# Kernel optimization log

Hardware: AMD Instinct MI355X
Metric: run time of the kernel (lower is better)

## Reference

```python
import jax, jax.numpy as jnp
import numpy as np

V = 8192        # variants
NREF = 262144   # total ref reads
NALT = 131072   # total alt reads
F_READ = 11     # tensors.NUM_READ_FEATURES
F_INFO = 9      # tensors.NUM_INFO_FEATURES
H = 256         # hidden width
MAX_ALT = 10


def setup_inputs() -> dict:
    key = jax.random.key(0)
    ks = jax.random.split(key, 24)
    p = lambda k, shp: (jax.random.normal(k, shp, dtype=jnp.float32) * 0.05)
    inp = {
        "reads": jax.random.normal(ks[0], (NREF + NALT, F_READ), dtype=jnp.float32),
        "info": jax.random.normal(ks[1], (V, F_INFO), dtype=jnp.float32),
        "ref_seg_ids": jnp.sort(jax.random.randint(ks[2], (NREF,), 0, V, dtype=jnp.int32)),
        "alt_seg_ids": jnp.sort(jax.random.randint(ks[3], (NALT,), 0, V, dtype=jnp.int32)),
        "variant_types": jax.random.randint(ks[4], (V,), 0, 3, dtype=jnp.int32),
        # phi: [F_READ, H, H]
        "phi_W0": p(ks[5], (F_READ, H)), "phi_b0": p(ks[6], (H,)),
        "phi_W1": p(ks[7], (H, H)), "phi_b1": p(ks[8], (H,)),
        # omega: [F_INFO, H]
        "om_W0": p(ks[9], (F_INFO, H)), "om_b0": p(ks[10], (H,)),
        # rho: [3H, H, H]
        "rho_W0": p(ks[11], (3 * H, H)), "rho_b0": p(ks[12], (H,)),
        "rho_W1": p(ks[13], (H, H)), "rho_b1": p(ks[14], (H,)),
        # 3 output MLPs, stacked: [H,H] -> [H,1]
        "out_W1": p(ks[15], (3, H, H)), "out_b1": p(ks[16], (3, H)),
        "out_W2": p(ks[17], (3, H, 1)), "out_b2": p(ks[18], (3, 1)),
        # calibration
        "conf": jnp.sqrt(jnp.arange(0, MAX_ALT + 1, dtype=jnp.float32)),
        "max_logit": jnp.array(10.0, dtype=jnp.float32),
    }
    return inp


def _seg_mean(x, seg_ids, num_segments):
    sums = jax.ops.segment_sum(x, seg_ids, num_segments=num_segments)
    counts = jax.ops.segment_sum(jnp.ones((x.shape[0],), x.dtype), seg_ids, num_segments=num_segments)
    return sums / jnp.maximum(counts, 1.0)[:, None], counts


def reference(reads, info, ref_seg_ids, alt_seg_ids, variant_types,
              phi_W0, phi_b0, phi_W1, phi_b1, om_W0, om_b0,
              rho_W0, rho_b0, rho_W1, rho_b1,
              out_W1, out_b1, out_W2, out_b2, conf, max_logit):
    lrelu = jax.nn.leaky_relu
    # phi MLP (leaky_relu between layers, none after last), then sigmoid
    h = lrelu(reads @ phi_W0 + phi_b0)
    phi_reads = jax.nn.sigmoid(h @ phi_W1 + phi_b1)          # [N, H]
    ref_reads = phi_reads[:NREF]
    alt_reads = phi_reads[NREF:]
    ref_means, _ = _seg_mean(ref_reads, ref_seg_ids, V)       # [V, H]
    alt_means, alt_counts = _seg_mean(alt_reads, alt_seg_ids, V)
    omega_info = jax.nn.sigmoid(info @ om_W0 + om_b0)         # [V, H]
    concat = jnp.concatenate([ref_means, alt_means, omega_info], axis=1)  # [V, 3H]
    agg = lrelu(concat @ rho_W0 + rho_b0) @ rho_W1 + rho_b1   # [V, H]
    # per-variant-type output MLPs, select by variant type
    o = lrelu(jnp.einsum('vd,tde->tve', agg, out_W1) + out_b1[:, None, :])
    outs = (jnp.einsum('tve,teo->tvo', o, out_W2) + out_b2[:, None, :])[:, :, 0]  # [3, V]
    logits = jnp.take_along_axis(outs, variant_types[None, :].astype(jnp.int32), axis=0)[0]
    # calibration
    trunc = jnp.minimum(alt_counts.astype(jnp.int32), MAX_ALT)
    logits = logits * conf[trunc]
    return max_logit * jnp.tanh(logits / max_logit)
```

## Files before the change

kernel.cpp:

```cpp
#include <hip/hip_runtime.h>
#include <cmath>

#define V 8192
#define NREF 262144
#define NALT 131072
#define NREADS (NREF + NALT)
#define FR 11
#define FI 9
#define HH 256
#define MAX_ALT 10

#define TILE_R 64
#define TILE_V 32

#define HPITCH 264
#define RBPITCH 40
#define CPITCH 776
#define APITCH 264

typedef short bf16x8 __attribute__((ext_vector_type(8)));
typedef float f32x4  __attribute__((ext_vector_type(4)));

__device__ __forceinline__ float sigmoidf_(float x) {
    return __builtin_amdgcn_rcpf(1.0f + __expf(-x));
}
__device__ __forceinline__ float lrelu_(float x) {
    return x > 0.0f ? x : 0.01f * x;
}
__device__ __forceinline__ unsigned short f2bf_(float f) {
    unsigned int u = __float_as_uint(f);
    u += 0x7FFFu + ((u >> 16) & 1u);
    return (unsigned short)(u >> 16);
}
__device__ __forceinline__ float bf2f_(unsigned short b) {
    return __uint_as_float(((unsigned int)b) << 16);
}

__global__ __launch_bounds__(256) void prep_kernel(
    const float* __restrict__ phi_W1, const float* __restrict__ rho_W0,
    const float* __restrict__ rho_W1, const float* __restrict__ out_W1,
    const float* __restrict__ phi_W0,
    unsigned short* __restrict__ w1t_phi, unsigned short* __restrict__ w0t,
    unsigned short* __restrict__ w1rt, unsigned short* __restrict__ whT,
    unsigned short* __restrict__ w0pT)
{
    __shared__ unsigned short sT[32][33];
    const int b = blockIdx.x;
    const int t = threadIdx.x;
    if (b < 512) {
        const float* src; unsigned short* dst; int R, C, bx, by;
        if (b < 64)       { src = phi_W1; dst = w1t_phi; R = 256; C = 256; bx = b & 7; by = b >> 3; }
        else if (b < 256) { int i = b - 64;  src = rho_W0; dst = w0t;  R = 768; C = 256; bx = i & 7; by = i >> 3; }
        else if (b < 320) { int i = b - 256; src = rho_W1; dst = w1rt; R = 256; C = 256; bx = i & 7; by = i >> 3; }
        else              { int i = b - 320; int z = i >> 6; i &= 63;
                            src = out_W1 + (size_t)z * HH * HH; dst = whT + (size_t)z * HH * HH;
                            R = 256; C = 256; bx = i & 7; by = i >> 3; }
        const int tx = t & 31, ty = t >> 5;
        const int r0 = by * 32, c0 = bx * 32;
#pragma unroll
        for (int k = 0; k < 4; k++)
            sT[ty + k * 8][tx] = f2bf_(src[(size_t)(r0 + ty + k * 8) * C + c0 + tx]);
        __syncthreads();
#pragma unroll
        for (int k = 0; k < 4; k++)
            dst[(size_t)(c0 + ty + k * 8) * R + r0 + tx] = sT[tx][ty + k * 8];
    } else {
        const int idx = (b - 512) * 256 + t;
        const int c = idx >> 5, k = idx & 31;
        unsigned short v = 0;
        if (k < FR) v = f2bf_(phi_W0[k * HH + c]);
        else if (k >= 16 && k < 16 + FR) v = f2bf_(phi_W0[(k - 16) * HH + c]);
        w0pT[idx] = v;
    }
}

__global__ __launch_bounds__(256, 4) void phi_seg_kernel(
    const float* __restrict__ reads,
    const int* __restrict__ ref_ids, const int* __restrict__ alt_ids,
    const unsigned short* __restrict__ w0pT, const float* __restrict__ b0,
    const unsigned short* __restrict__ w1t, const float* __restrict__ b1,
    float* __restrict__ ref_sums, float* __restrict__ alt_sums,
    int* __restrict__ ref_cnt, int* __restrict__ alt_cnt)
{
    __shared__ __align__(16) unsigned short sH[TILE_R * HPITCH];
    __shared__ __align__(16) unsigned short sRB[TILE_R * RBPITCH];

    const int t  = threadIdx.x;
    const int r0 = blockIdx.x * TILE_R;
    const bool is_ref = (r0 < NREF);
    const int* seg_ids = is_ref ? ref_ids : alt_ids;
    const int sbase    = is_ref ? r0 : (r0 - NREF);
    float* sums = is_ref ? ref_sums : alt_sums;
    int*   cnts = is_ref ? ref_cnt  : alt_cnt;

    {
        const int row = t >> 2, q = t & 3;
        const float* rp = reads + (size_t)(r0 + row) * FR;
        unsigned short o[8];
        if (q == 0) {
#pragma unroll
            for (int j = 0; j < 8; j++) o[j] = f2bf_(rp[j]);
        } else if (q == 1) {
#pragma unroll
            for (int j = 0; j < 8; j++) o[j] = (j < 3) ? f2bf_(rp[8 + j]) : 0;
        } else if (q == 2) {
#pragma unroll
            for (int j = 0; j < 8; j++) {
                float f = rp[j];
                o[j] = f2bf_(f - bf2f_(f2bf_(f)));
            }
        } else {
#pragma unroll
            for (int j = 0; j < 8; j++) {
                if (j < 3) { float f = rp[8 + j]; o[j] = f2bf_(f - bf2f_(f2bf_(f))); }
                else o[j] = 0;
            }
        }
        uint4 pk;
        pk.x = (unsigned int)o[0] | ((unsigned int)o[1] << 16);
        pk.y = (unsigned int)o[2] | ((unsigned int)o[3] << 16);
        pk.z = (unsigned int)o[4] | ((unsigned int)o[5] << 16);
        pk.w = (unsigned int)o[6] | ((unsigned int)o[7] << 16);
        *(uint4*)&sRB[row * RBPITCH + q * 8] = pk;
    }
    __syncthreads();

    const int wv   = t >> 6;
    const int lane = t & 63;
    const int lrow = lane & 15;
    const int quad = lane >> 4;

    bf16x8 aw[4], br[4];
#pragma unroll
    for (int cm = 0; cm < 4; cm++)
        aw[cm] = *(const bf16x8*)(w0pT + ((wv * 64 + cm * 16 + lrow) << 5) + quad * 8);
#pragma unroll
    for (int rt = 0; rt < 4; rt++)
        br[rt] = *(const bf16x8*)&sRB[(rt * 16 + lrow) * RBPITCH + quad * 8];

    f32x4 c1[4][4];
#pragma unroll
    for (int cm = 0; cm < 4; cm++)
#pragma unroll
        for (int rt = 0; rt < 4; rt++)
            c1[cm][rt] = __builtin_amdgcn_mfma_f32_16x16x32_bf16(
                aw[cm], br[rt], (f32x4){0.f, 0.f, 0.f, 0.f}, 0, 0, 0);

#pragma unroll
    for (int cm = 0; cm < 4; cm++) {
        const float4 bias = *(const float4*)(b0 + wv * 64 + cm * 16 + quad * 4);
#pragma unroll
        for (int rt = 0; rt < 4; rt++) {
            const int r = rt * 16 + lrow;
            unsigned int p01 =
                (unsigned int)f2bf_(lrelu_(c1[cm][rt][0] + bias.x)) |
                ((unsigned int)f2bf_(lrelu_(c1[cm][rt][1] + bias.y)) << 16);
            unsigned int p23 =
                (unsigned int)f2bf_(lrelu_(c1[cm][rt][2] + bias.z)) |
                ((unsigned int)f2bf_(lrelu_(c1[cm][rt][3] + bias.w)) << 16);
            uint2 pk = {p01, p23};
            *(uint2*)&sH[r * HPITCH + wv * 64 + cm * 16 + quad * 4] = pk;
        }
    }
    __syncthreads();

    f32x4 acc[4][4];
#pragma unroll
    for (int mt = 0; mt < 4; mt++)
#pragma unroll
        for (int nt = 0; nt < 4; nt++)
            acc[mt][nt] = (f32x4){0.f, 0.f, 0.f, 0.f};

#pragma unroll
    for (int kk = 0; kk < 8; kk++) {
        bf16x8 am[4], bn[4];
#pragma unroll
        for (int mt = 0; mt < 4; mt++)
            am[mt] = *(const bf16x8*)&sH[(mt * 16 + lrow) * HPITCH + kk * 32 + quad * 8];
#pragma unroll
        for (int nt = 0; nt < 4; nt++)
            bn[nt] = *(const bf16x8*)(w1t + (size_t)(wv * 64 + nt * 16 + lrow) * HH + kk * 32 + quad * 8);
#pragma unroll
        for (int mt = 0; mt < 4; mt++)
#pragma unroll
            for (int nt = 0; nt < 4; nt++)
                acc[mt][nt] = __builtin_amdgcn_mfma_f32_16x16x32_bf16(
                    am[mt], bn[nt], acc[mt][nt], 0, 0, 0);
    }

#pragma unroll
    for (int nt = 0; nt < 4; nt++) {
        const float bb = b1[wv * 64 + nt * 16 + lrow];
#pragma unroll
        for (int mt = 0; mt < 4; mt++)
#pragma unroll
            for (int r = 0; r < 4; r++)
                acc[mt][nt][r] = sigmoidf_(acc[mt][nt][r] + bb);
    }

    const int myseg = seg_ids[sbase + lane];
    const int prev  = __shfl_up(myseg, 1);
    const bool flag = (lane == 0) || (myseg != prev);
    unsigned long long m = __ballot(flag);

    while (m) {
        const int start = (int)__builtin_ctzll(m);
        const unsigned long long m2 = m & (m - 1);
        const int end = m2 ? (int)__builtin_ctzll(m2) : 64;
        m = m2;
        const int seg = __shfl(myseg, start);

        float msk[4][4];
#pragma unroll
        for (int mt = 0; mt < 4; mt++)
#pragma unroll
            for (int r = 0; r < 4; r++) {
                const int row = mt * 16 + quad * 4 + r;
                msk[mt][r] = (row >= start && row < end) ? 1.0f : 0.0f;
            }
#pragma unroll
        for (int nt = 0; nt < 4; nt++) {
            float s = 0.f;
#pragma unroll
            for (int mt = 0; mt < 4; mt++)
#pragma unroll
                for (int r = 0; r < 4; r++)
                    s = fmaf(acc[mt][nt][r], msk[mt][r], s);
            s += __shfl_down(s, 32);
            s += __shfl_down(s, 16);
            if (quad == 0)
                atomicAdd(&sums[(size_t)seg * HH + wv * 64 + nt * 16 + lrow], s);
        }
        if (t == 0) atomicAdd(&cnts[seg], end - start);
    }
}

__global__ __launch_bounds__(1024, 1) void rho_mfma_kernel(
    const float* __restrict__ info, const int* __restrict__ vtypes,
    const float* __restrict__ om_W0, const float* __restrict__ om_b0,
    const unsigned short* __restrict__ w0t, const float* __restrict__ rho_b0,
    const unsigned short* __restrict__ w1rt, const float* __restrict__ rho_b1,
    const unsigned short* __restrict__ whT, const float* __restrict__ out_b1,
    const float* __restrict__ out_W2, const float* __restrict__ out_b2,
    const float* __restrict__ conf, const float* __restrict__ max_logit,
    const float* __restrict__ ref_sums, const float* __restrict__ alt_sums,
    const int* __restrict__ ref_cnt, const int* __restrict__ alt_cnt,
    float* __restrict__ out)
{
    __shared__ __align__(16) unsigned short sC[TILE_V * CPITCH];
    __shared__ __align__(16) float sInfo[TILE_V][12];
    __shared__ float sRinvR[TILE_V], sRinvA[TILE_V];
    __shared__ float sPart[16][3][TILE_V];

    unsigned short* sA1  = sC;
    unsigned short* sAgg = sC + TILE_V * APITCH;

    const int t  = threadIdx.x;
    const int v0 = blockIdx.x * TILE_V;

    if (t < TILE_V) {
        sRinvR[t] = __builtin_amdgcn_rcpf(fmaxf((float)ref_cnt[v0 + t], 1.0f));
        sRinvA[t] = __builtin_amdgcn_rcpf(fmaxf((float)alt_cnt[v0 + t], 1.0f));
    }
    for (int idx = t; idx < TILE_V * FI; idx += 1024) {
        int i = idx / FI, k = idx - i * FI;
        sInfo[i][k] = info[(size_t)(v0 + i) * FI + k];
    }
    __syncthreads();

    {
        const int c = t & 255, grp = t >> 8;
        float om0r[FI];
#pragma unroll
        for (int k = 0; k < FI; k++) om0r[k] = om_W0[k * HH + c];
        const float omb = om_b0[c];
#pragma unroll
        for (int ii = 0; ii < 8; ii++) {
            const int i = grp * 8 + ii, v = v0 + i;
            float rm = ref_sums[(size_t)v * HH + c] * sRinvR[i];
            float am = alt_sums[(size_t)v * HH + c] * sRinvA[i];
            float a = omb;
#pragma unroll
            for (int k = 0; k < FI; k++) a = fmaf(sInfo[i][k], om0r[k], a);
            sC[i * CPITCH + c]          = f2bf_(rm);
            sC[i * CPITCH + HH + c]     = f2bf_(am);
            sC[i * CPITCH + 2 * HH + c] = f2bf_(sigmoidf_(a));
        }
    }
    __syncthreads();

    const int wv   = t >> 6;
    const int lane = t & 63;
    const int lrow = lane & 15;
    const int quad = lane >> 4;
    const int ncol = wv * 16 + lrow;

    f32x4 p1[2] = {(f32x4){0.f,0.f,0.f,0.f}, (f32x4){0.f,0.f,0.f,0.f}};
#pragma unroll 4
    for (int kk = 0; kk < 24; kk++) {
        bf16x8 a0 = *(const bf16x8*)&sC[lrow * CPITCH + kk * 32 + quad * 8];
        bf16x8 a1 = *(const bf16x8*)&sC[(16 + lrow) * CPITCH + kk * 32 + quad * 8];
        bf16x8 bn = *(const bf16x8*)(w0t + (size_t)ncol * 768 + kk * 32 + quad * 8);
        p1[0] = __builtin_amdgcn_mfma_f32_16x16x32_bf16(a0, bn, p1[0], 0, 0, 0);
        p1[1] = __builtin_amdgcn_mfma_f32_16x16x32_bf16(a1, bn, p1[1], 0, 0, 0);
    }
    __syncthreads();
    {
        const float bb = rho_b0[ncol];
#pragma unroll
        for (int mt = 0; mt < 2; mt++)
#pragma unroll
            for (int r = 0; r < 4; r++) {
                const int row = mt * 16 + quad * 4 + r;
                sA1[row * APITCH + ncol] = f2bf_(lrelu_(p1[mt][r] + bb));
            }
    }
    __syncthreads();

    f32x4 p2[2] = {(f32x4){0.f,0.f,0.f,0.f}, (f32x4){0.f,0.f,0.f,0.f}};
#pragma unroll
    for (int kk = 0; kk < 8; kk++) {
        bf16x8 a0 = *(const bf16x8*)&sA1[lrow * APITCH + kk * 32 + quad * 8];
        bf16x8 a1 = *(const bf16x8*)&sA1[(16 + lrow) * APITCH + kk * 32 + quad * 8];
        bf16x8 bn = *(const bf16x8*)(w1rt + (size_t)ncol * HH + kk * 32 + quad * 8);
        p2[0] = __builtin_amdgcn_mfma_f32_16x16x32_bf16(a0, bn, p2[0], 0, 0, 0);
        p2[1] = __builtin_amdgcn_mfma_f32_16x16x32_bf16(a1, bn, p2[1], 0, 0, 0);
    }
    {
        const float bb = rho_b1[ncol];
#pragma unroll
        for (int mt = 0; mt < 2; mt++)
#pragma unroll
            for (int r = 0; r < 4; r++) {
                const int row = mt * 16 + quad * 4 + r;
                sAgg[row * APITCH + ncol] = f2bf_(p2[mt][r] + bb);
            }
    }
    __syncthreads();

    bf16x8 aF[8][2];
#pragma unroll
    for (int kk = 0; kk < 8; kk++)
#pragma unroll
        for (int mt = 0; mt < 2; mt++)
            aF[kk][mt] = *(const bf16x8*)&sAgg[(mt * 16 + lrow) * APITCH + kk * 32 + quad * 8];

    for (int h = 0; h < 3; h++) {
        f32x4 p3[2] = {(f32x4){0.f,0.f,0.f,0.f}, (f32x4){0.f,0.f,0.f,0.f}};
#pragma unroll
        for (int kk = 0; kk < 8; kk++) {
            bf16x8 bn = *(const bf16x8*)(whT + ((size_t)h * HH + ncol) * HH + kk * 32 + quad * 8);
            p3[0] = __builtin_amdgcn_mfma_f32_16x16x32_bf16(aF[kk][0], bn, p3[0], 0, 0, 0);
            p3[1] = __builtin_amdgcn_mfma_f32_16x16x32_bf16(aF[kk][1], bn, p3[1], 0, 0, 0);
        }
        const float bb = out_b1[h * HH + ncol];
        const float w2 = out_W2[h * HH + ncol];
#pragma unroll
        for (int mt = 0; mt < 2; mt++)
#pragma unroll
            for (int r = 0; r < 4; r++) {
                float v = lrelu_(p3[mt][r] + bb) * w2;
                v += __shfl_down(v, 8);
                v += __shfl_down(v, 4);
                v += __shfl_down(v, 2);
                v += __shfl_down(v, 1);
                if (lrow == 0) sPart[wv][h][mt * 16 + quad * 4 + r] = v;
            }
    }
    __syncthreads();

    if (t < TILE_V) {
        const int v = v0 + t;
        const int ty = vtypes[v];
        float logit = 0.f;
#pragma unroll
        for (int w = 0; w < 16; w++) logit += sPart[w][ty][t];
        logit += out_b2[ty];
        const int tr = min(alt_cnt[v], MAX_ALT);
        logit *= conf[tr];
        const float ml = max_logit[0];
        out[v] = ml * tanhf(logit / ml);
    }
}

extern "C" void kernel_launch(void* const* d_in, const int* in_sizes, int n_in,
                              void* d_out, int out_size, void* d_ws, size_t ws_size,
                              hipStream_t stream) {
    const float* reads    = (const float*)d_in[0];
    const float* info     = (const float*)d_in[1];
    const int*   ref_ids  = (const int*)d_in[2];
    const int*   alt_ids  = (const int*)d_in[3];
    const int*   vtypes   = (const int*)d_in[4];
    const float* phi_W0   = (const float*)d_in[5];
    const float* phi_b0   = (const float*)d_in[6];
    const float* phi_W1   = (const float*)d_in[7];
    const float* phi_b1   = (const float*)d_in[8];
    const float* om_W0    = (const float*)d_in[9];
    const float* om_b0    = (const float*)d_in[10];
    const float* rho_W0   = (const float*)d_in[11];
    const float* rho_b0   = (const float*)d_in[12];
    const float* rho_W1   = (const float*)d_in[13];
    const float* rho_b1   = (const float*)d_in[14];
    const float* out_W1   = (const float*)d_in[15];
    const float* out_b1   = (const float*)d_in[16];
    const float* out_W2   = (const float*)d_in[17];
    const float* out_b2   = (const float*)d_in[18];
    const float* conf     = (const float*)d_in[19];
    const float* max_lg   = (const float*)d_in[20];
    float* out = (float*)d_out;

    float* ref_sums = (float*)d_ws;
    float* alt_sums = ref_sums + (size_t)V * HH;
    int*   ref_cnt  = (int*)(alt_sums + (size_t)V * HH);
    int*   alt_cnt  = ref_cnt + V;
    unsigned short* w1t_phi = (unsigned short*)(alt_cnt + V);
    unsigned short* w0t     = w1t_phi + (size_t)HH * HH;
    unsigned short* w1rt    = w0t + (size_t)HH * 768;
    unsigned short* whT     = w1rt + (size_t)HH * HH;
    unsigned short* w0pT    = whT + (size_t)3 * HH * HH;

    const size_t zero_bytes = (size_t)2 * V * HH * sizeof(float) + (size_t)2 * V * sizeof(int);
    hipMemsetAsync(d_ws, 0, zero_bytes, stream);

    prep_kernel<<<544, 256, 0, stream>>>(phi_W1, rho_W0, rho_W1, out_W1, phi_W0,
                                         w1t_phi, w0t, w1rt, whT, w0pT);

    phi_seg_kernel<<<NREADS / TILE_R, 256, 0, stream>>>(
        reads, ref_ids, alt_ids, w0pT, phi_b0, w1t_phi, phi_b1,
        ref_sums, alt_sums, ref_cnt, alt_cnt);

    rho_mfma_kernel<<<V / TILE_V, 1024, 0, stream>>>(
        info, vtypes, om_W0, om_b0, w0t, rho_b0, w1rt, rho_b1,
        whT, out_b1, out_W2, out_b2, conf, max_lg,
        ref_sums, alt_sums, ref_cnt, alt_cnt, out);
}
```

Measured before the change: 264.3 us.

## Retile rho kernel to 16 variants per 512-thread block with two columns per wave

The rho/output kernel now handles 16 variants per block with 512 threads, and each wave computes two 16-column N tiles that share one A fragment, instead of two M tiles sharing one B fragment. This doubles the grid to 512 blocks and allows several blocks per CU, aiming to improve occupancy and latency hiding. The cost is that each block re-reads the full weight matrices from global/L2 for half as many variants, so weight traffic roughly doubles. The phi kernel also switches read staging to a row/quarter mapping with fewer branches, and packs bf16 conversions with the hardware paired-conversion intrinsic.

```diff
diff --git a/kernel.cpp b/kernel.cpp
--- a/kernel.cpp
+++ b/kernel.cpp
@@ -1,4 +1,5 @@
 #include <hip/hip_runtime.h>
+#include <hip/hip_bf16.h>
 #include <cmath>
 
 #define V 8192
@@ -11,7 +12,7 @@
 #define MAX_ALT 10
 
 #define TILE_R 64
-#define TILE_V 32
+#define TILE_V 16
 
 #define HPITCH 264
 #define RBPITCH 40
@@ -34,6 +35,11 @@
 }
 __device__ __forceinline__ float bf2f_(unsigned short b) {
     return __uint_as_float(((unsigned int)b) << 16);
+}
+__device__ __forceinline__ unsigned int pk2bf_(float a, float b) {
+    union { __hip_bfloat162 h2; unsigned int u; } cvt;
+    cvt.h2 = __float22bfloat162_rn(make_float2(a, b));
+    return cvt.u;
 }
 
 __global__ __launch_bounds__(256) void prep_kernel(
@@ -94,26 +100,19 @@
     int*   cnts = is_ref ? ref_cnt  : alt_cnt;
 
     {
-        const int row = t >> 2, q = t & 3;
+        const int row = t & 63, q = t >> 6;
         const float* rp = reads + (size_t)(r0 + row) * FR;
+        const int nj = (q & 1) ? 3 : 8;
+        const int cb = (q & 1) ? 8 : 0;
         unsigned short o[8];
-        if (q == 0) {
-#pragma unroll
-            for (int j = 0; j < 8; j++) o[j] = f2bf_(rp[j]);
-        } else if (q == 1) {
-#pragma unroll
-            for (int j = 0; j < 8; j++) o[j] = (j < 3) ? f2bf_(rp[8 + j]) : 0;
-        } else if (q == 2) {
-#pragma unroll
-            for (int j = 0; j < 8; j++) {
-                float f = rp[j];
+#pragma unroll
+        for (int j = 0; j < 8; j++) o[j] = 0;
+        if (q < 2) {
+            for (int j = 0; j < nj; j++) o[j] = f2bf_(rp[cb + j]);
+        } else {
+            for (int j = 0; j < nj; j++) {
+                float f = rp[cb + j];
                 o[j] = f2bf_(f - bf2f_(f2bf_(f)));
-            }
-        } else {
-#pragma unroll
-            for (int j = 0; j < 8; j++) {
-                if (j < 3) { float f = rp[8 + j]; o[j] = f2bf_(f - bf2f_(f2bf_(f))); }
-                else o[j] = 0;
             }
         }
         uint4 pk;
@@ -152,13 +151,9 @@
 #pragma unroll
         for (int rt = 0; rt < 4; rt++) {
             const int r = rt * 16 + lrow;
-            unsigned int p01 =
-                (unsigned int)f2bf_(lrelu_(c1[cm][rt][0] + bias.x)) |
-                ((unsigned int)f2bf_(lrelu_(c1[cm][rt][1] + bias.y)) << 16);
-            unsigned int p23 =
-                (unsigned int)f2bf_(lrelu_(c1[cm][rt][2] + bias.z)) |
-                ((unsigned int)f2bf_(lrelu_(c1[cm][rt][3] + bias.w)) << 16);
-            uint2 pk = {p01, p23};
+            uint2 pk;
+            pk.x = pk2bf_(lrelu_(c1[cm][rt][0] + bias.x), lrelu_(c1[cm][rt][1] + bias.y));
+            pk.y = pk2bf_(lrelu_(c1[cm][rt][2] + bias.z), lrelu_(c1[cm][rt][3] + bias.w));
             *(uint2*)&sH[r * HPITCH + wv * 64 + cm * 16 + quad * 4] = pk;
         }
     }
@@ -209,6 +204,7 @@
         const int end = m2 ? (int)__builtin_ctzll(m2) : 64;
         m = m2;
         const int seg = __shfl(myseg, start);
+        float* srow = sums + (size_t)seg * HH + wv * 64;
 
         float msk[4][4];
 #pragma unroll
@@ -229,13 +225,13 @@
             s += __shfl_down(s, 32);
             s += __shfl_down(s, 16);
             if (quad == 0)
-                atomicAdd(&sums[(size_t)seg * HH + wv * 64 + nt * 16 + lrow], s);
+                atomicAdd(&srow[nt * 16 + lrow], s);
         }
         if (t == 0) atomicAdd(&cnts[seg], end - start);
     }
 }
 
-__global__ __launch_bounds__(1024, 1) void rho_mfma_kernel(
+__global__ __launch_bounds__(512, 4) void rho_mfma_kernel(
     const float* __restrict__ info, const int* __restrict__ vtypes,
     const float* __restrict__ om_W0, const float* __restrict__ om_b0,
     const unsigned short* __restrict__ w0t, const float* __restrict__ rho_b0,
@@ -250,7 +246,7 @@
     __shared__ __align__(16) unsigned short sC[TILE_V * CPITCH];
     __shared__ __align__(16) float sInfo[TILE_V][12];
     __shared__ float sRinvR[TILE_V], sRinvA[TILE_V];
-    __shared__ float sPart[16][3][TILE_V];
+    __shared__ float sPart[8][3][TILE_V];
 
     unsigned short* sA1  = sC;
     unsigned short* sAgg = sC + TILE_V * APITCH;
@@ -262,7 +258,7 @@
         sRinvR[t] = __builtin_amdgcn_rcpf(fmaxf((float)ref_cnt[v0 + t], 1.0f));
         sRinvA[t] = __builtin_amdgcn_rcpf(fmaxf((float)alt_cnt[v0 + t], 1.0f));
     }
-    for (int idx = t; idx < TILE_V * FI; idx += 1024) {
+    for (int idx = t; idx < TILE_V * FI; idx += 512) {
         int i = idx / FI, k = idx - i * FI;
         sInfo[i][k] = info[(size_t)(v0 + i) * FI + k];
     }
@@ -293,79 +289,75 @@
     const int lane = t & 63;
     const int lrow = lane & 15;
     const int quad = lane >> 4;
-    const int ncol = wv * 16 + lrow;
+    const int nc0  = wv * 32 + lrow;
+    const int nc1  = nc0 + 16;
 
     f32x4 p1[2] = {(f32x4){0.f,0.f,0.f,0.f}, (f32x4){0.f,0.f,0.f,0.f}};
 #pragma unroll 4
     for (int kk = 0; kk < 24; kk++) {
-        bf16x8 a0 = *(const bf16x8*)&sC[lrow * CPITCH + kk * 32 + quad * 8];
-        bf16x8 a1 = *(const bf16x8*)&sC[(16 + lrow) * CPITCH + kk * 32 + quad * 8];
-        bf16x8 bn = *(const bf16x8*)(w0t + (size_t)ncol * 768 + kk * 32 + quad * 8);
-        p1[0] = __builtin_amdgcn_mfma_f32_16x16x32_bf16(a0, bn, p1[0], 0, 0, 0);
-        p1[1] = __builtin_amdgcn_mfma_f32_16x16x32_bf16(a1, bn, p1[1], 0, 0, 0);
+        bf16x8 a  = *(const bf16x8*)&sC[lrow * CPITCH + kk * 32 + quad * 8];
+        bf16x8 b0_ = *(const bf16x8*)(w0t + (size_t)nc0 * 768 + kk * 32 + quad * 8);
+        bf16x8 b1_ = *(const bf16x8*)(w0t + (size_t)nc1 * 768 + kk * 32 + quad * 8);
+        p1[0] = __builtin_amdgcn_mfma_f32_16x16x32_bf16(a, b0_, p1[0], 0, 0, 0);
+        p1[1] = __builtin_amdgcn_mfma_f32_16x16x32_bf16(a, b1_, p1[1], 0, 0, 0);
     }
     __syncthreads();
     {
-        const float bb = rho_b0[ncol];
-#pragma unroll
-        for (int mt = 0; mt < 2; mt++)
-#pragma unroll
-            for (int r = 0; r < 4; r++) {
-                const int row = mt * 16 + quad * 4 + r;
-                sA1[row * APITCH + ncol] = f2bf_(lrelu_(p1[mt][r] + bb));
-            }
+        const float bb0 = rho_b0[nc0], bb1 = rho_b0[nc1];
+#pragma unroll
+        for (int r = 0; r < 4; r++) {
+            const int row = quad * 4 + r;
+            sA1[row * APITCH + nc0] = f2bf_(lrelu_(p1[0][r] + bb0));
+            sA1[row * APITCH + nc1] = f2bf_(lrelu_(p1[1][r] + bb1));
+        }
     }
     __syncthreads();
 
     f32x4 p2[2] = {(f32x4){0.f,0.f,0.f,0.f}, (f32x4){0.f,0.f,0.f,0.f}};
 #pragma unroll
     for (int kk = 0; kk < 8; kk++) {
-        bf16x8 a0 = *(const bf16x8*)&sA1[lrow * APITCH + kk * 32 + quad * 8];
-        bf16x8 a1 = *(const bf16x8*)&sA1[(16 + lrow) * APITCH + kk * 32 + quad * 8];
-        bf16x8 bn = *(const bf16x8*)(w1rt + (size_t)ncol * HH + kk * 32 + quad * 8);
-        p2[0] = __builtin_amdgcn_mfma_f32_16x16x32_bf16(a0, bn, p2[0], 0, 0, 0);
-        p2[1] = __builtin_amdgcn_mfma_f32_16x16x32_bf16(a1, bn, p2[1], 0, 0, 0);
+        bf16x8 a  = *(const bf16x8*)&sA1[lrow * APITCH + kk * 32 + quad * 8];
+        bf16x8 b0_ = *(const bf16x8*)(w1rt + (size_t)nc0 * HH + kk * 32 + quad * 8);
+        bf16x8 b1_ = *(const bf16x8*)(w1rt + (size_t)nc1 * HH + kk * 32 + quad * 8);
+        p2[0] = __builtin_amdgcn_mfma_f32_16x16x32_bf16(a, b0_, p2[0], 0, 0, 0);
+        p2[1] = __builtin_amdgcn_mfma_f32_16x16x32_bf16(a, b1_, p2[1], 0, 0, 0);
     }
     {
-        const float bb = rho_b1[ncol];
-#pragma unroll
-        for (int mt = 0; mt < 2; mt++)
-#pragma unroll
-            for (int r = 0; r < 4; r++) {
-                const int row = mt * 16 + quad * 4 + r;
-                sAgg[row * APITCH + ncol] = f2bf_(p2[mt][r] + bb);
-            }
-    }
-    __syncthreads();
-
-    bf16x8 aF[8][2];
+        const float bb0 = rho_b1[nc0], bb1 = rho_b1[nc1];
+#pragma unroll
+        for (int r = 0; r < 4; r++) {
+            const int row = quad * 4 + r;
+            sAgg[row * APITCH + nc0] = f2bf_(p2[0][r] + bb0);
+            sAgg[row * APITCH + nc1] = f2bf_(p2[1][r] + bb1);
+        }
+    }
+    __syncthreads();
+
+    bf16x8 aF[8];
 #pragma unroll
     for (int kk = 0; kk < 8; kk++)
-#pragma unroll
-        for (int mt = 0; mt < 2; mt++)
-            aF[kk][mt] = *(const bf16x8*)&sAgg[(mt * 16 + lrow) * APITCH + kk * 32 + quad * 8];
+        aF[kk] = *(const bf16x8*)&sAgg[lrow * APITCH + kk * 32 + quad * 8];
 
     for (int h = 0; h < 3; h++) {
         f32x4 p3[2] = {(f32x4){0.f,0.f,0.f,0.f}, (f32x4){0.f,0.f,0.f,0.f}};
 #pragma unroll
         for (int kk = 0; kk < 8; kk++) {
-            bf16x8 bn = *(const bf16x8*)(whT + ((size_t)h * HH + ncol) * HH + kk * 32 + quad * 8);
-            p3[0] = __builtin_amdgcn_mfma_f32_16x16x32_bf16(aF[kk][0], bn, p3[0], 0, 0, 0);
-            p3[1] = __builtin_amdgcn_mfma_f32_16x16x32_bf16(aF[kk][1], bn, p3[1], 0, 0, 0);
-        }
-        const float bb = out_b1[h * HH + ncol];
-        const float w2 = out_W2[h * HH + ncol];
-#pragma unroll
-        for (int mt = 0; mt < 2; mt++)
-#pragma unroll
-            for (int r = 0; r < 4; r++) {
-                float v = lrelu_(p3[mt][r] + bb) * w2;
-                v += __shfl_down(v, 8);
-                v += __shfl_down(v, 4);
-                v += __shfl_down(v, 2);
-                v += __shfl_down(v, 1);
-                if (lrow == 0) sPart[wv][h][mt * 16 + quad * 4 + r] = v;
-            }
+            bf16x8 b0_ = *(const bf16x8*)(whT + ((size_t)h * HH + nc0) * HH + kk * 32 + quad * 8);
+            bf16x8 b1_ = *(const bf16x8*)(whT + ((size_t)h * HH + nc1) * HH + kk * 32 + quad * 8);
+            p3[0] = __builtin_amdgcn_mfma_f32_16x16x32_bf16(aF[kk], b0_, p3[0], 0, 0, 0);
+            p3[1] = __builtin_amdgcn_mfma_f32_16x16x32_bf16(aF[kk], b1_, p3[1], 0, 0, 0);
+        }
+        const float bbA = out_b1[h * HH + nc0], bbB = out_b1[h * HH + nc1];
+        const float w2A = out_W2[h * HH + nc0], w2B = out_W2[h * HH + nc1];
+#pragma unroll
+        for (int r = 0; r < 4; r++) {
+            float v = lrelu_(p3[0][r] + bbA) * w2A + lrelu_(p3[1][r] + bbB) * w2B;
+            v += __shfl_down(v, 8);
+            v += __shfl_down(v, 4);
+            v += __shfl_down(v, 2);
+            v += __shfl_down(v, 1);
+            if (lrow == 0) sPart[wv][h][quad * 4 + r] = v;
+        }
     }
     __syncthreads();
 
@@ -374,7 +366,7 @@
         const int ty = vtypes[v];
         float logit = 0.f;
 #pragma unroll
-        for (int w = 0; w < 16; w++) logit += sPart[w][ty][t];
+        for (int w = 0; w < 8; w++) logit += sPart[w][ty][t];
         logit += out_b2[ty];
         const int tr = min(alt_cnt[v], MAX_ALT);
         logit *= conf[tr];
@@ -429,7 +421,7 @@
         reads, ref_ids, alt_ids, w0pT, phi_b0, w1t_phi, phi_b1,
         ref_sums, alt_sums, ref_cnt, alt_cnt);
 
-    rho_mfma_kernel<<<V / TILE_V, 1024, 0, stream>>>(
+    rho_mfma_kernel<<<V / TILE_V, 512, 0, stream>>>(
         info, vtypes, om_W0, om_b0, w0t, rho_b0, w1rt, rho_b1,
         whT, out_b1, out_W2, out_b2, conf, max_lg,
         ref_sums, alt_sums, ref_cnt, alt_cnt, out);
```

After: 288.4 us. 9.1% more time.

## Double phi row tile to 128 with 512-thread blocks and 32-column wave slices

Applied to the files above, without the earlier changes.

The phi/segment kernel now processes 128 reads per block with 8 waves, each owning 32 output columns across all 128 rows instead of 64 columns over 64 rows. This halves how often the phi_W1 weights are fetched from global memory per read, so weight traffic per read drops. It also switches to a packed bf16x2 conversion intrinsic. In exchange, the shared-memory footprint per block doubles and occupancy per CU may change. The segment reduction is also split into two 64-row passes, which issues more atomics per segment boundary.

```diff
diff --git a/kernel.cpp b/kernel.cpp
--- a/kernel.cpp
+++ b/kernel.cpp
@@ -1,4 +1,5 @@
 #include <hip/hip_runtime.h>
+#include <hip/hip_bf16.h>
 #include <cmath>
 
 #define V 8192
@@ -10,7 +11,7 @@
 #define HH 256
 #define MAX_ALT 10
 
-#define TILE_R 64
+#define TILE_R 128
 #define TILE_V 32
 
 #define HPITCH 264
@@ -34,6 +35,11 @@
 }
 __device__ __forceinline__ float bf2f_(unsigned short b) {
     return __uint_as_float(((unsigned int)b) << 16);
+}
+__device__ __forceinline__ unsigned int pk2bf_(float a, float b) {
+    union { __hip_bfloat162 h2; unsigned int u; } cvt;
+    cvt.h2 = __float22bfloat162_rn(make_float2(a, b));
+    return cvt.u;
 }
 
 __global__ __launch_bounds__(256) void prep_kernel(
@@ -74,7 +80,7 @@
     }
 }
 
-__global__ __launch_bounds__(256, 4) void phi_seg_kernel(
+__global__ __launch_bounds__(512, 2) void phi_seg_kernel(
     const float* __restrict__ reads,
     const int* __restrict__ ref_ids, const int* __restrict__ alt_ids,
     const unsigned short* __restrict__ w0pT, const float* __restrict__ b0,
@@ -94,26 +100,19 @@
     int*   cnts = is_ref ? ref_cnt  : alt_cnt;
 
     {
-        const int row = t >> 2, q = t & 3;
+        const int row = t & 127, q = t >> 7;
         const float* rp = reads + (size_t)(r0 + row) * FR;
+        const int nj = (q & 1) ? 3 : 8;
+        const int cb = (q & 1) ? 8 : 0;
         unsigned short o[8];
-        if (q == 0) {
-#pragma unroll
-            for (int j = 0; j < 8; j++) o[j] = f2bf_(rp[j]);
-        } else if (q == 1) {
-#pragma unroll
-            for (int j = 0; j < 8; j++) o[j] = (j < 3) ? f2bf_(rp[8 + j]) : 0;
-        } else if (q == 2) {
-#pragma unroll
-            for (int j = 0; j < 8; j++) {
-                float f = rp[j];
+#pragma unroll
+        for (int j = 0; j < 8; j++) o[j] = 0;
+        if (q < 2) {
+            for (int j = 0; j < nj; j++) o[j] = f2bf_(rp[cb + j]);
+        } else {
+            for (int j = 0; j < nj; j++) {
+                float f = rp[cb + j];
                 o[j] = f2bf_(f - bf2f_(f2bf_(f)));
-            }
-        } else {
-#pragma unroll
-            for (int j = 0; j < 8; j++) {
-                if (j < 3) { float f = rp[8 + j]; o[j] = f2bf_(f - bf2f_(f2bf_(f))); }
-                else o[j] = 0;
             }
         }
         uint4 pk;
@@ -130,108 +129,101 @@
     const int lrow = lane & 15;
     const int quad = lane >> 4;
 
-    bf16x8 aw[4], br[4];
-#pragma unroll
-    for (int cm = 0; cm < 4; cm++)
-        aw[cm] = *(const bf16x8*)(w0pT + ((wv * 64 + cm * 16 + lrow) << 5) + quad * 8);
-#pragma unroll
-    for (int rt = 0; rt < 4; rt++)
-        br[rt] = *(const bf16x8*)&sRB[(rt * 16 + lrow) * RBPITCH + quad * 8];
-
-    f32x4 c1[4][4];
-#pragma unroll
-    for (int cm = 0; cm < 4; cm++)
-#pragma unroll
-        for (int rt = 0; rt < 4; rt++)
-            c1[cm][rt] = __builtin_amdgcn_mfma_f32_16x16x32_bf16(
-                aw[cm], br[rt], (f32x4){0.f, 0.f, 0.f, 0.f}, 0, 0, 0);
-
-#pragma unroll
-    for (int cm = 0; cm < 4; cm++) {
-        const float4 bias = *(const float4*)(b0 + wv * 64 + cm * 16 + quad * 4);
-#pragma unroll
-        for (int rt = 0; rt < 4; rt++) {
-            const int r = rt * 16 + lrow;
-            unsigned int p01 =
-                (unsigned int)f2bf_(lrelu_(c1[cm][rt][0] + bias.x)) |
-                ((unsigned int)f2bf_(lrelu_(c1[cm][rt][1] + bias.y)) << 16);
-            unsigned int p23 =
-                (unsigned int)f2bf_(lrelu_(c1[cm][rt][2] + bias.z)) |
-                ((unsigned int)f2bf_(lrelu_(c1[cm][rt][3] + bias.w)) << 16);
-            uint2 pk = {p01, p23};
-            *(uint2*)&sH[r * HPITCH + wv * 64 + cm * 16 + quad * 4] = pk;
-        }
-    }
-    __syncthreads();
-
-    f32x4 acc[4][4];
-#pragma unroll
-    for (int mt = 0; mt < 4; mt++)
-#pragma unroll
-        for (int nt = 0; nt < 4; nt++)
+    {
+        bf16x8 br[8];
+#pragma unroll
+        for (int rt = 0; rt < 8; rt++)
+            br[rt] = *(const bf16x8*)&sRB[(rt * 16 + lrow) * RBPITCH + quad * 8];
+
+#pragma unroll
+        for (int cm = 0; cm < 2; cm++) {
+            const bf16x8 aw = *(const bf16x8*)(w0pT + ((wv * 32 + cm * 16 + lrow) << 5) + quad * 8);
+            f32x4 c1[8];
+#pragma unroll
+            for (int rt = 0; rt < 8; rt++)
+                c1[rt] = __builtin_amdgcn_mfma_f32_16x16x32_bf16(
+                    aw, br[rt], (f32x4){0.f, 0.f, 0.f, 0.f}, 0, 0, 0);
+
+            const float4 bias = *(const float4*)(b0 + wv * 32 + cm * 16 + quad * 4);
+#pragma unroll
+            for (int rt = 0; rt < 8; rt++) {
+                const int r = rt * 16 + lrow;
+                uint2 pk;
+                pk.x = pk2bf_(lrelu_(c1[rt][0] + bias.x), lrelu_(c1[rt][1] + bias.y));
+                pk.y = pk2bf_(lrelu_(c1[rt][2] + bias.z), lrelu_(c1[rt][3] + bias.w));
+                *(uint2*)&sH[r * HPITCH + wv * 32 + cm * 16 + quad * 4] = pk;
+            }
+        }
+    }
+    __syncthreads();
+
+    f32x4 acc[8][2];
+#pragma unroll
+    for (int mt = 0; mt < 8; mt++)
+#pragma unroll
+        for (int nt = 0; nt < 2; nt++)
             acc[mt][nt] = (f32x4){0.f, 0.f, 0.f, 0.f};
 
 #pragma unroll
     for (int kk = 0; kk < 8; kk++) {
-        bf16x8 am[4], bn[4];
-#pragma unroll
-        for (int mt = 0; mt < 4; mt++)
-            am[mt] = *(const bf16x8*)&sH[(mt * 16 + lrow) * HPITCH + kk * 32 + quad * 8];
-#pragma unroll
-        for (int nt = 0; nt < 4; nt++)
-            bn[nt] = *(const bf16x8*)(w1t + (size_t)(wv * 64 + nt * 16 + lrow) * HH + kk * 32 + quad * 8);
-#pragma unroll
-        for (int mt = 0; mt < 4; mt++)
-#pragma unroll
-            for (int nt = 0; nt < 4; nt++)
-                acc[mt][nt] = __builtin_amdgcn_mfma_f32_16x16x32_bf16(
-                    am[mt], bn[nt], acc[mt][nt], 0, 0, 0);
-    }
-
-#pragma unroll
-    for (int nt = 0; nt < 4; nt++) {
-        const float bb = b1[wv * 64 + nt * 16 + lrow];
-#pragma unroll
-        for (int mt = 0; mt < 4; mt++)
+        const bf16x8 bn0 = *(const bf16x8*)(w1t + (size_t)(wv * 32 + lrow) * HH + kk * 32 + quad * 8);
+        const bf16x8 bn1 = *(const bf16x8*)(w1t + (size_t)(wv * 32 + 16 + lrow) * HH + kk * 32 + quad * 8);
+#pragma unroll
+        for (int mt = 0; mt < 8; mt++) {
+            const bf16x8 am = *(const bf16x8*)&sH[(mt * 16 + lrow) * HPITCH + kk * 32 + quad * 8];
+            acc[mt][0] = __builtin_amdgcn_mfma_f32_16x16x32_bf16(am, bn0, acc[mt][0], 0, 0, 0);
+            acc[mt][1] = __builtin_amdgcn_mfma_f32_16x16x32_bf16(am, bn1, acc[mt][1], 0, 0, 0);
+        }
+    }
+
+#pragma unroll
+    for (int nt = 0; nt < 2; nt++) {
+        const float bb = b1[wv * 32 + nt * 16 + lrow];
+#pragma unroll
+        for (int mt = 0; mt < 8; mt++)
 #pragma unroll
             for (int r = 0; r < 4; r++)
                 acc[mt][nt][r] = sigmoidf_(acc[mt][nt][r] + bb);
     }
 
-    const int myseg = seg_ids[sbase + lane];
-    const int prev  = __shfl_up(myseg, 1);
-    const bool flag = (lane == 0) || (myseg != prev);
-    unsigned long long m = __ballot(flag);
-
-    while (m) {
-        const int start = (int)__builtin_ctzll(m);
-        const unsigned long long m2 = m & (m - 1);
-        const int end = m2 ? (int)__builtin_ctzll(m2) : 64;
-        m = m2;
-        const int seg = __shfl(myseg, start);
-
-        float msk[4][4];
-#pragma unroll
-        for (int mt = 0; mt < 4; mt++)
-#pragma unroll
-            for (int r = 0; r < 4; r++) {
-                const int row = mt * 16 + quad * 4 + r;
-                msk[mt][r] = (row >= start && row < end) ? 1.0f : 0.0f;
-            }
-#pragma unroll
-        for (int nt = 0; nt < 4; nt++) {
-            float s = 0.f;
-#pragma unroll
-            for (int mt = 0; mt < 4; mt++)
-#pragma unroll
-                for (int r = 0; r < 4; r++)
-                    s = fmaf(acc[mt][nt][r], msk[mt][r], s);
-            s += __shfl_down(s, 32);
-            s += __shfl_down(s, 16);
-            if (quad == 0)
-                atomicAdd(&sums[(size_t)seg * HH + wv * 64 + nt * 16 + lrow], s);
-        }
-        if (t == 0) atomicAdd(&cnts[seg], end - start);
+#pragma unroll
+    for (int g = 0; g < 2; g++) {
+        const int myseg = seg_ids[sbase + g * 64 + lane];
+        const int prev  = __shfl_up(myseg, 1);
+        const bool flag = (lane == 0) || (myseg != prev);
+        unsigned long long m = __ballot(flag);
+
+        while (m) {
+            const int start = (int)__builtin_ctzll(m);
+            const unsigned long long m2 = m & (m - 1);
+            const int end = m2 ? (int)__builtin_ctzll(m2) : 64;
+            m = m2;
+            const int seg = __shfl(myseg, start);
+            float* srow = sums + (size_t)seg * HH + wv * 32;
+
+            float msk[4][4];
+#pragma unroll
+            for (int lm = 0; lm < 4; lm++)
+#pragma unroll
+                for (int r = 0; r < 4; r++) {
+                    const int lrw = lm * 16 + quad * 4 + r;
+                    msk[lm][r] = (lrw >= start && lrw < end) ? 1.0f : 0.0f;
+                }
+#pragma unroll
+            for (int nt = 0; nt < 2; nt++) {
+                float s = 0.f;
+#pragma unroll
+                for (int lm = 0; lm < 4; lm++)
+#pragma unroll
+                    for (int r = 0; r < 4; r++)
+                        s = fmaf(acc[g * 4 + lm][nt][r], msk[lm][r], s);
+                s += __shfl_down(s, 32);
+                s += __shfl_down(s, 16);
+                if (quad == 0)
+                    atomicAdd(&srow[nt * 16 + lrow], s);
+            }
+            if (t == 0) atomicAdd(&cnts[seg], end - start);
+        }
     }
 }
 
@@ -425,7 +417,7 @@
     prep_kernel<<<544, 256, 0, stream>>>(phi_W1, rho_W0, rho_W1, out_W1, phi_W0,
                                          w1t_phi, w0t, w1rt, whT, w0pT);
 
-    phi_seg_kernel<<<NREADS / TILE_R, 256, 0, stream>>>(
+    phi_seg_kernel<<<NREADS / TILE_R, 512, 0, stream>>>(
         reads, ref_ids, alt_ids, w0pT, phi_b0, w1t_phi, phi_b1,
         ref_sums, alt_sums, ref_cnt, alt_cnt);
 
```

New measurement: 249.9 us. -5.4%, faster.
